# Kernel optimization log

Measured on AMD Instinct MI355X. Metric: run time of the kernel, lower is better.

## Reference

```python
import jax, jax.numpy as jnp
import numpy as np

F = 26  # num_sparse_features
N = F + 1
# upper-triangular (offset=1) index pairs, matching torch.triu_indices(N, N, offset=1)
_TRIU_I, _TRIU_J = np.triu_indices(N, k=1)


def setup_inputs() -> dict:
    key = jax.random.key(0)
    k1, k2 = jax.random.split(key)
    B, D = 16384, 128
    dense_features = jax.random.normal(k1, (B, D), dtype=jnp.float32)
    sparse_features = jax.random.normal(k2, (B, F, D), dtype=jnp.float32)
    return {"dense_features": dense_features, "sparse_features": sparse_features}


def reference(dense_features, sparse_features):
    # combined: [B, N, D] with N = F + 1 (dense row first)
    combined = jnp.concatenate([dense_features[:, None, :], sparse_features], axis=1)
    # pairwise dot products: [B, N, N]
    interactions = jnp.einsum('bnd,bmd->bnm', combined, combined)
    # gather strict upper triangle: [B, N*(N-1)/2]
    interactions_flat = interactions[:, _TRIU_I, _TRIU_J]
    # output: [B, D + F + F choose 2]
    return jnp.concatenate([dense_features, interactions_flat], axis=1)
```

## Files before the change

kernel.cpp:

```cpp
#include <hip/hip_runtime.h>


#define FEAT 26
#define NROW 27
#define DDIM 128
#define NTRI 351
#define OUTW 479
#define LDST 136
#define WPB   4
#define GRID  1024
#define NWAVE (GRID * WPB)
#define ITERS 4

typedef _Float16 half2v __attribute__((ext_vector_type(2)));
typedef _Float16 half4v __attribute__((ext_vector_type(4)));
typedef _Float16 half8v __attribute__((ext_vector_type(8)));
typedef float    f32x16 __attribute__((ext_vector_type(16)));

#define LGKM0() __builtin_amdgcn_s_waitcnt(0xC07F)

__global__ __launch_bounds__(256) void interaction_kernel(
    const float* __restrict__ dense,
    const float* __restrict__ sparse,
    float* __restrict__ out)
{
    __shared__ _Float16 Xs[WPB][32][LDST];
    __shared__ float    Tri[WPB][NTRI + 1];

    const int lane = threadIdx.x & 63;
    const int w    = threadIdx.x >> 6;
    const int gw   = blockIdx.x * WPB + w;

    const int j0 = lane & 31;
    const int q  = lane >> 5;
    const half8v* fp = (const half8v*)(&Xs[w][j0][q * 8]);

    for (int it = 0; it < ITERS; ++it) {
        const long b = gw + (long)it * NWAVE;
        const float* dn   = dense  + b * DDIM;
        const float* sp   = sparse + b * (FEAT * DDIM);
        float*       orow = out    + b * OUTW;

        {
            float2 v = *(const float2*)(dn + lane * 2);
            orow[lane * 2 + 0] = v.x;
            orow[lane * 2 + 1] = v.y;
            half2v h;
            h.x = (_Float16)v.x; h.y = (_Float16)v.y;
            *(half2v*)(&Xs[w][0][lane * 2]) = h;
        }

#pragma unroll
        for (int t = 0; t < 13; ++t) {
            int idx = t * 64 + lane;
            float4 v = *(const float4*)(sp + idx * 4);
            int row = 1 + (idx >> 5);
            int col = (idx & 31) * 4;
            half4v h;
            h.x = (_Float16)v.x; h.y = (_Float16)v.y;
            h.z = (_Float16)v.z; h.w = (_Float16)v.w;
            *(half4v*)(&Xs[w][row][col]) = h;
        }
        __builtin_amdgcn_wave_barrier();
        LGKM0();

        f32x16 acc = {0,0,0,0,0,0,0,0,0,0,0,0,0,0,0,0};
#pragma unroll
        for (int s = 0; s < 8; ++s) {
            half8v f = fp[2 * s];
            acc = __builtin_amdgcn_mfma_f32_32x32x16_f16(f, f, acc, 0, 0, 0);
        }

#pragma unroll
        for (int reg = 0; reg < 16; ++reg) {
            int row = (reg & 3) + 8 * (reg >> 2) + 4 * q;
            if (row < j0 && j0 < NROW) {
                int t = row * (2 * NROW - row - 1) / 2 + (j0 - row - 1);
                Tri[w][t] = acc[reg];
            }
        }
        __builtin_amdgcn_wave_barrier();
        LGKM0();

#pragma unroll
        for (int t = 0; t < 6; ++t) {
            int idx = t * 64 + lane;
            if (idx < NTRI) orow[DDIM + idx] = Tri[w][idx];
        }
        __builtin_amdgcn_wave_barrier();
    }
}

extern "C" void kernel_launch(void* const* d_in, const int* in_sizes, int n_in,
                              void* d_out, int out_size, void* d_ws, size_t ws_size,
                              hipStream_t stream) {
    const float* dense  = (const float*)d_in[0];
    const float* sparse = (const float*)d_in[1];
    float* out = (float*)d_out;
    interaction_kernel<<<GRID, 256, 0, stream>>>(dense, sparse, out);
}
```

Baseline: 311.9 us.

## Load MFMA operands directly from global memory, skipping LDS staging

Each lane now loads its own row of the combined matrix straight from global memory into registers in MFMA fragment layout and converts it to fp16, instead of staging the data through a shared-memory tile. Lanes for rows 27-31 are clamped to reuse the last sparse row, so those loads are redundant but stay in bounds. This removes the LDS writes, reads and the wave barrier, and the grid is doubled with half as many iterations per wave. The cost is a less coalesced global access pattern (each lane reads 32-byte chunks strided across rows) and more live registers for the fragments.

After: 310.4 us. No clear change (-0.5%).

```diff
diff --git a/kernel.cpp b/kernel.cpp
--- a/kernel.cpp
+++ b/kernel.cpp
@@ -6,14 +6,11 @@
 #define DDIM 128
 #define NTRI 351
 #define OUTW 479
-#define LDST 136
 #define WPB   4
-#define GRID  1024
+#define GRID  2048
 #define NWAVE (GRID * WPB)
-#define ITERS 4
+#define ITERS 2
 
-typedef _Float16 half2v __attribute__((ext_vector_type(2)));
-typedef _Float16 half4v __attribute__((ext_vector_type(4)));
 typedef _Float16 half8v __attribute__((ext_vector_type(8)));
 typedef float    f32x16 __attribute__((ext_vector_type(16)));
 
@@ -24,16 +21,15 @@
     const float* __restrict__ sparse,
     float* __restrict__ out)
 {
-    __shared__ _Float16 Xs[WPB][32][LDST];
-    __shared__ float    Tri[WPB][NTRI + 1];
+    __shared__ float Tri[WPB][NTRI + 1];
 
     const int lane = threadIdx.x & 63;
     const int w    = threadIdx.x >> 6;
     const int gw   = blockIdx.x * WPB + w;
 
-    const int j0 = lane & 31;
+    const int r  = lane & 31;
     const int q  = lane >> 5;
-    const half8v* fp = (const half8v*)(&Xs[w][j0][q * 8]);
+    const int rr = (r > FEAT) ? FEAT : r;
 
     for (int it = 0; it < ITERS; ++it) {
         const long b = gw + (long)it * NWAVE;
@@ -41,45 +37,41 @@
         const float* sp   = sparse + b * (FEAT * DDIM);
         float*       orow = out    + b * OUTW;
 
+        const float* rowp = (rr == 0) ? dn : (sp + (rr - 1) * DDIM);
+
+        half8v fr[8];
+#pragma unroll
+        for (int s = 0; s < 8; ++s) {
+            const float* p = rowp + s * 16 + q * 8;
+            float4 a = *(const float4*)(p);
+            float4 c = *(const float4*)(p + 4);
+            half8v f;
+            f[0] = (_Float16)a.x; f[1] = (_Float16)a.y;
+            f[2] = (_Float16)a.z; f[3] = (_Float16)a.w;
+            f[4] = (_Float16)c.x; f[5] = (_Float16)c.y;
+            f[6] = (_Float16)c.z; f[7] = (_Float16)c.w;
+            fr[s] = f;
+        }
+
         {
             float2 v = *(const float2*)(dn + lane * 2);
             orow[lane * 2 + 0] = v.x;
             orow[lane * 2 + 1] = v.y;
-            half2v h;
-            h.x = (_Float16)v.x; h.y = (_Float16)v.y;
-            *(half2v*)(&Xs[w][0][lane * 2]) = h;
         }
-
-#pragma unroll
-        for (int t = 0; t < 13; ++t) {
-            int idx = t * 64 + lane;
-            float4 v = *(const float4*)(sp + idx * 4);
-            int row = 1 + (idx >> 5);
-            int col = (idx & 31) * 4;
-            half4v h;
-            h.x = (_Float16)v.x; h.y = (_Float16)v.y;
-            h.z = (_Float16)v.z; h.w = (_Float16)v.w;
-            *(half4v*)(&Xs[w][row][col]) = h;
-        }
-        __builtin_amdgcn_wave_barrier();
-        LGKM0();
 
         f32x16 acc = {0,0,0,0,0,0,0,0,0,0,0,0,0,0,0,0};
 #pragma unroll
-        for (int s = 0; s < 8; ++s) {
-            half8v f = fp[2 * s];
-            acc = __builtin_amdgcn_mfma_f32_32x32x16_f16(f, f, acc, 0, 0, 0);
-        }
+        for (int s = 0; s < 8; ++s)
+            acc = __builtin_amdgcn_mfma_f32_32x32x16_f16(fr[s], fr[s], acc, 0, 0, 0);
 
 #pragma unroll
         for (int reg = 0; reg < 16; ++reg) {
             int row = (reg & 3) + 8 * (reg >> 2) + 4 * q;
-            if (row < j0 && j0 < NROW) {
-                int t = row * (2 * NROW - row - 1) / 2 + (j0 - row - 1);
+            if (row < r && r < NROW) {
+                int t = row * (2 * NROW - row - 1) / 2 + (r - row - 1);
                 Tri[w][t] = acc[reg];
             }
         }
-        __builtin_amdgcn_wave_barrier();
         LGKM0();
 
 #pragma unroll
```
